# Performance work log

Measured on AMD Instinct MI355X. Metric: run time of the kernel, lower is better.

The kernel has to match this reference:

```python
import jax, jax.numpy as jnp
import numpy as np

KEY_DIM = 128
TEMPERATURE = float(np.sqrt(KEY_DIM))


def setup_inputs() -> dict:
    key = jax.random.key(0)
    kq, kk, kv = jax.random.split(key, 3)
    B, S, D = 32, 2048, KEY_DIM
    q = jax.random.normal(kq, (B, S, D), dtype=jnp.float32)
    k = jax.random.normal(kk, (B, S, D), dtype=jnp.float32)
    v = jax.random.normal(kv, (B, S, D), dtype=jnp.float32)
    return {"q": q, "k": k, "v": v}


def reference(q, k, v):
    # energies: [B, S, S] = q @ k^T / sqrt(D)
    energies = jnp.einsum("bqd,bkd->bqk", q, k) / TEMPERATURE
    S = energies.shape[1]
    # causal mask: disallow attending to future positions (strict upper triangle)
    causal = jnp.tril(jnp.ones((S, S), dtype=bool))
    energies = jnp.where(causal[None, :, :], energies, -jnp.inf)
    attention = jax.nn.softmax(energies, axis=2)  # dropout p=0 -> identity
    context = jnp.einsum("bqk,bkd->bqd", attention, v)
    return (context, attention)
```

## Files before the change

kernel.cpp:

```cpp
#include <hip/hip_runtime.h>


#define BATCH 32
#define SEQ 2048
#define DIM 128
#define BQ 64
#define NT 32
#define NTHREADS 256
#define SCALE 0.08838834764831845f

typedef __attribute__((ext_vector_type(8))) short short8;
typedef __attribute__((ext_vector_type(4))) short short4v;
typedef __attribute__((ext_vector_type(4))) float floatx4;

#define QP 136
#define PP 72

__device__ __forceinline__ short f2bf(float x) {
  unsigned u = __builtin_bit_cast(unsigned, x);
  u += 0x7fffu + ((u >> 16) & 1u);
  return (short)(u >> 16);
}
__device__ __forceinline__ float bf2f(short s) {
  return __builtin_bit_cast(float, (unsigned)(unsigned short)s << 16);
}

__device__ __forceinline__ void stage_f32(const float* __restrict__ g,
                                          short* __restrict__ lds, int tid) {
  int r = tid >> 2, c0 = tid & 3;
  const float* grow = g + r * DIM;
  short* lrow = lds + r * QP;
#pragma unroll
  for (int i = 0; i < 8; ++i) {
    int dq = c0 + 4 * i;
    floatx4 val = *(const floatx4*)(grow + dq * 4);
    short4v o;
    o.x = f2bf(val.x); o.y = f2bf(val.y); o.z = f2bf(val.z); o.w = f2bf(val.w);
    *(short4v*)(lrow + dq * 4) = o;
  }
}
__device__ __forceinline__ void stage_vT_f32(const float* __restrict__ g,
                                             short* __restrict__ lds, int tid) {
  int r = tid >> 2, c0 = tid & 3;
  const float* grow = g + r * DIM;
#pragma unroll
  for (int i = 0; i < 8; ++i) {
    int dq = c0 + 4 * i;
    floatx4 val = *(const floatx4*)(grow + dq * 4);
    lds[(dq * 4 + 0) * PP + r] = f2bf(val.x);
    lds[(dq * 4 + 1) * PP + r] = f2bf(val.y);
    lds[(dq * 4 + 2) * PP + r] = f2bf(val.z);
    lds[(dq * 4 + 3) * PP + r] = f2bf(val.w);
  }
}
__device__ __forceinline__ void load_k_regs(const short* __restrict__ src,
                                            int tid, short8* kr) {
#pragma unroll
  for (int i = 0; i < 4; ++i) {
    int idx = tid + i * 256;
    int r = idx >> 4, g = idx & 15;
    kr[i] = *(const short8*)(src + r * DIM + g * 8);
  }
}
__device__ __forceinline__ void write_k_regs(const short8* kr,
                                             short* __restrict__ ks, int tid) {
#pragma unroll
  for (int i = 0; i < 4; ++i) {
    int idx = tid + i * 256;
    int r = idx >> 4, g = idx & 15;
    *(short8*)(ks + r * QP + g * 8) = kr[i];
  }
}
__device__ __forceinline__ void load_v_regs(const short* __restrict__ src,
                                            int tid, short8* vr) {
#pragma unroll
  for (int i = 0; i < 4; ++i) {
    int idx = tid + i * 256;
    int d = idx >> 3, g = idx & 7;
    vr[i] = *(const short8*)(src + (size_t)d * SEQ + g * 8);
  }
}
__device__ __forceinline__ void write_v_regs(const short8* vr,
                                             short* __restrict__ vts, int tid) {
#pragma unroll
  for (int i = 0; i < 4; ++i) {
    int idx = tid + i * 256;
    int d = idx >> 3, g = idx & 7;
    *(short8*)(vts + d * PP + g * 8) = vr[i];
  }
}

__global__ __launch_bounds__(NTHREADS) void convert_kv(
    const float* __restrict__ k, const float* __restrict__ v,
    short* __restrict__ kbf, short* __restrict__ vbf) {
  int blk = blockIdx.x, tid = threadIdx.x;
  if (blk < BATCH * NT) {
    __shared__ short vt[DIM * PP];
    int b = blk >> 5, s0 = (blk & 31) * BQ;
    const float* src = v + ((size_t)b * SEQ + s0) * DIM;
    int r = tid >> 2, c0 = tid & 3;
#pragma unroll
    for (int i = 0; i < 8; ++i) {
      int dq = c0 + 4 * i;
      floatx4 val = *(const floatx4*)(src + (size_t)r * DIM + dq * 4);
      vt[(dq * 4 + 0) * PP + r] = f2bf(val.x);
      vt[(dq * 4 + 1) * PP + r] = f2bf(val.y);
      vt[(dq * 4 + 2) * PP + r] = f2bf(val.z);
      vt[(dq * 4 + 3) * PP + r] = f2bf(val.w);
    }
    __syncthreads();
#pragma unroll
    for (int i = 0; i < 4; ++i) {
      int idx = tid + i * 256;
      int d = idx >> 3, g = idx & 7;
      *(short8*)(vbf + ((size_t)b * DIM + d) * SEQ + s0 + g * 8) =
          *(const short8*)(vt + d * PP + g * 8);
    }
  } else {
    size_t base = (size_t)(blk - BATCH * NT) * 4096;
    const floatx4* src = (const floatx4*)k;
#pragma unroll
    for (int i = 0; i < 16; ++i) {
      size_t idx = base + i * 256 + tid;
      floatx4 val = src[idx];
      short4v o;
      o.x = f2bf(val.x); o.y = f2bf(val.y); o.z = f2bf(val.z); o.w = f2bf(val.w);
      *(short4v*)(kbf + idx * 4) = o;
    }
  }
}

template <bool PRE>
__global__ __launch_bounds__(NTHREADS, 2) void attn_fused(
    const float* __restrict__ q, const float* __restrict__ k,
    const float* __restrict__ v, const short* __restrict__ kbf,
    const short* __restrict__ vbf, float* __restrict__ ctx,
    float* __restrict__ attn) {
  __shared__ short ks[BQ * QP];
  __shared__ short rest[18432];
  short* vts = rest;
  short* psA = rest + DIM * PP;
  short* psB = psA + BQ * PP;

  const int tid = threadIdx.x;
  const int i = blockIdx.x;
  const int xcd = i & 7;
  const int jj = i >> 3;
  const int b = xcd + 8 * (jj >> 4);
  const int pr = jj & 15;
  const int qtA = pr, qtB = 31 - pr;

  const float* qbase = q + (size_t)b * SEQ * DIM;
  const short* kb = PRE ? kbf + (size_t)b * SEQ * DIM : nullptr;
  const short* vb = PRE ? vbf + (size_t)b * DIM * SEQ : nullptr;
  const float* kbase = k + (size_t)b * SEQ * DIM;
  const float* vbase = v + (size_t)b * SEQ * DIM;
  float* ctxA = ctx + ((size_t)b * SEQ + qtA * BQ) * DIM;
  float* ctxB = ctx + ((size_t)b * SEQ + qtB * BQ) * DIM;
  float* attnA = attn + ((size_t)b * SEQ + qtA * BQ) * SEQ;
  float* attnB = attn + ((size_t)b * SEQ + qtB * BQ) * SEQ;

  stage_f32(qbase + (size_t)qtA * BQ * DIM, rest, tid);
  stage_f32(qbase + (size_t)qtB * BQ * DIM, rest + BQ * QP, tid);

  const int lane = tid & 63;
  const int w = tid >> 6;
  const int quad = lane >> 4;
  const int c = lane & 15;

  __syncthreads();
  short8 afA[4], afB[4];
  {
    const short* ra = rest + (w * 16 + c) * QP + quad * 8;
    const short* rb = ra + BQ * QP;
#pragma unroll
    for (int kk = 0; kk < 4; ++kk) {
      afA[kk] = *(const short8*)(ra + kk * 32);
      afB[kk] = *(const short8*)(rb + kk * 32);
    }
  }

  const int lrow_lo = w * 16 + quad * 4;
  const int nIt = qtB + 1;
  const int zcA = (qtA + 1) * BQ, nzA4 = (SEQ - zcA) >> 2;
  const int zcB = (qtB + 1) * BQ, nzB4 = (SEQ - zcB) >> 2;
  const floatx4 z4 = {0.f, 0.f, 0.f, 0.f};

  float plA[4] = {0.f, 0.f, 0.f, 0.f}, plB[4] = {0.f, 0.f, 0.f, 0.f};
  if (PRE) {
    short8 kr[4];
    load_k_regs(kb, tid, kr);
    write_k_regs(kr, ks, tid);
  } else {
    stage_f32(kbase, ks, tid);
  }
  __syncthreads();
  for (int kt = 0; kt < nIt; ++kt) {
    short* cur = (kt & 1) ? rest : ks;
    short* nxt = (kt & 1) ? ks : rest;
    const bool more = (kt + 1 < nIt);
    short8 kr[4];
    if (PRE && more) load_k_regs(kb + (size_t)(kt + 1) * BQ * DIM, tid, kr);

    const bool activeA = (kt <= qtA);
    const bool diagB = (kt == qtB), diagA = (kt == qtA);
#pragma unroll
    for (int nt = 0; nt < 4; ++nt) {
      const short* brow = cur + (nt * 16 + c) * QP + quad * 8;
      short8 bf[4];
#pragma unroll
      for (int kk = 0; kk < 4; ++kk) bf[kk] = *(const short8*)(brow + kk * 32);
      floatx4 aB = {0.f, 0.f, 0.f, 0.f};
#pragma unroll
      for (int kk = 0; kk < 4; ++kk)
        aB = __builtin_amdgcn_mfma_f32_16x16x32_bf16(afB[kk], bf[kk], aB, 0, 0, 0);
#pragma unroll
      for (int r = 0; r < 4; ++r) {
        bool msk = diagB && (nt * 16 + c > lrow_lo + r);
        plB[r] += msk ? 0.f : __expf(aB[r] * SCALE);
      }
      if (activeA) {
        floatx4 aA = {0.f, 0.f, 0.f, 0.f};
#pragma unroll
        for (int kk = 0; kk < 4; ++kk)
          aA = __builtin_amdgcn_mfma_f32_16x16x32_bf16(afA[kk], bf[kk], aA, 0, 0, 0);
#pragma unroll
        for (int r = 0; r < 4; ++r) {
          bool msk = diagA && (nt * 16 + c > lrow_lo + r);
          plA[r] += msk ? 0.f : __expf(aA[r] * SCALE);
        }
      }
    }

    {
      int r0 = (kt * BQ) / nIt, r1 = ((kt + 1) * BQ) / nIt;
      for (int r = r0; r < r1; ++r) {
        float* rowpA = attnA + (size_t)r * SEQ + zcA;
        for (int c4 = tid; c4 < nzA4; c4 += NTHREADS) *(floatx4*)(rowpA + c4 * 4) = z4;
        float* rowpB = attnB + (size_t)r * SEQ + zcB;
        for (int c4 = tid; c4 < nzB4; c4 += NTHREADS) *(floatx4*)(rowpB + c4 * 4) = z4;
      }
    }

    if (more) {
      if (PRE) write_k_regs(kr, nxt, tid);
      else stage_f32(kbase + (size_t)(kt + 1) * BQ * DIM, nxt, tid);
    }
    __syncthreads();
  }

  float invlA[4], invlB[4];
#pragma unroll
  for (int r = 0; r < 4; ++r) {
#pragma unroll
    for (int off = 1; off < 16; off <<= 1) {
      plA[r] += __shfl_xor(plA[r], off, 16);
      plB[r] += __shfl_xor(plB[r], off, 16);
    }
    invlA[r] = 1.f / plA[r];
    invlB[r] = 1.f / plB[r];
  }

  floatx4 oaccA[8], oaccB[8];
#pragma unroll
  for (int nt = 0; nt < 8; ++nt) { oaccA[nt] = (floatx4)(0.f); oaccB[nt] = (floatx4)(0.f); }

  const short* prowA = psA + (w * 16 + c) * PP + quad * 8;
  const short* prowB = psB + (w * 16 + c) * PP + quad * 8;

  short8 kr2[4], vr2[4];
  if (PRE) { load_k_regs(kb, tid, kr2); load_v_regs(vb, tid, vr2); }
  for (int kt = 0; kt < nIt; ++kt) {
    __syncthreads();
    if (PRE) {
      write_k_regs(kr2, ks, tid);
      write_v_regs(vr2, vts, tid);
    } else {
      stage_f32(kbase + (size_t)kt * BQ * DIM, ks, tid);
      stage_vT_f32(vbase + (size_t)kt * BQ * DIM, vts, tid);
    }
    __syncthreads();
    const bool more = (kt + 1 < nIt);
    if (PRE && more) {
      load_k_regs(kb + (size_t)(kt + 1) * BQ * DIM, tid, kr2);
      load_v_regs(vb + (size_t)(kt + 1) * BQ, tid, vr2);
    }

    const bool activeA = (kt <= qtA);
    const bool diagB = (kt == qtB), diagA = (kt == qtA);
#pragma unroll
    for (int nt = 0; nt < 4; ++nt) {
      const short* brow = ks + (nt * 16 + c) * QP + quad * 8;
      short8 bf[4];
#pragma unroll
      for (int kk = 0; kk < 4; ++kk) bf[kk] = *(const short8*)(brow + kk * 32);
      floatx4 aB = {0.f, 0.f, 0.f, 0.f};
#pragma unroll
      for (int kk = 0; kk < 4; ++kk)
        aB = __builtin_amdgcn_mfma_f32_16x16x32_bf16(afB[kk], bf[kk], aB, 0, 0, 0);
#pragma unroll
      for (int r = 0; r < 4; ++r) {
        bool msk = diagB && (nt * 16 + c > lrow_lo + r);
        float p = msk ? 0.f : __expf(aB[r] * SCALE) * invlB[r];
        psB[(lrow_lo + r) * PP + nt * 16 + c] = f2bf(p);
      }
      if (activeA) {
        floatx4 aA = {0.f, 0.f, 0.f, 0.f};
#pragma unroll
        for (int kk = 0; kk < 4; ++kk)
          aA = __builtin_amdgcn_mfma_f32_16x16x32_bf16(afA[kk], bf[kk], aA, 0, 0, 0);
#pragma unroll
        for (int r = 0; r < 4; ++r) {
          bool msk = diagA && (nt * 16 + c > lrow_lo + r);
          float p = msk ? 0.f : __expf(aA[r] * SCALE) * invlA[r];
          psA[(lrow_lo + r) * PP + nt * 16 + c] = f2bf(p);
        }
      }
    }

#pragma unroll
    for (int ks2 = 0; ks2 < 2; ++ks2) {
      short8 paB = *(const short8*)(prowB + ks2 * 32);
      short8 paA;
      if (activeA) paA = *(const short8*)(prowA + ks2 * 32);
#pragma unroll
      for (int nt = 0; nt < 8; ++nt) {
        short8 vf = *(const short8*)(vts + (nt * 16 + c) * PP + ks2 * 32 + quad * 8);
        oaccB[nt] = __builtin_amdgcn_mfma_f32_16x16x32_bf16(paB, vf, oaccB[nt], 0, 0, 0);
        if (activeA)
          oaccA[nt] = __builtin_amdgcn_mfma_f32_16x16x32_bf16(paA, vf, oaccA[nt], 0, 0, 0);
      }
    }

#pragma unroll
    for (int it = 0; it < 4; ++it) {
      int idx = lane + it * 64;
      int r = (idx >> 4) + w * 16;
      int q4 = idx & 15;
      short4v pb = *(const short4v*)(psB + r * PP + q4 * 4);
      floatx4 fo;
      fo.x = bf2f(pb.x); fo.y = bf2f(pb.y); fo.z = bf2f(pb.z); fo.w = bf2f(pb.w);
      *(floatx4*)(attnB + (size_t)r * SEQ + kt * BQ + q4 * 4) = fo;
      if (activeA) {
        short4v pa = *(const short4v*)(psA + r * PP + q4 * 4);
        floatx4 fa;
        fa.x = bf2f(pa.x); fa.y = bf2f(pa.y); fa.z = bf2f(pa.z); fa.w = bf2f(pa.w);
        *(floatx4*)(attnA + (size_t)r * SEQ + kt * BQ + q4 * 4) = fa;
      }
    }
  }

#pragma unroll
  for (int nt = 0; nt < 8; ++nt)
#pragma unroll
    for (int r = 0; r < 4; ++r) {
      ctxA[(size_t)(lrow_lo + r) * DIM + nt * 16 + c] = oaccA[nt][r];
      ctxB[(size_t)(lrow_lo + r) * DIM + nt * 16 + c] = oaccB[nt][r];
    }
}

extern "C" void kernel_launch(void* const* d_in, const int* in_sizes, int n_in,
                              void* d_out, int out_size, void* d_ws, size_t ws_size,
                              hipStream_t stream) {
  (void)in_sizes; (void)n_in; (void)out_size;
  const float* q = (const float*)d_in[0];
  const float* k = (const float*)d_in[1];
  const float* v = (const float*)d_in[2];
  float* ctx = (float*)d_out;
  float* attn = ctx + (size_t)BATCH * SEQ * DIM;
  const size_t kv_elems = (size_t)BATCH * SEQ * DIM;
  const size_t need = kv_elems * 2 * sizeof(short);
  dim3 grid(BATCH * NT / 2);
  if (ws_size >= need) {
    short* kbf = (short*)d_ws;
    short* vbf = kbf + kv_elems;
    convert_kv<<<dim3(BATCH * NT + 512), NTHREADS, 0, stream>>>(k, v, kbf, vbf);
    attn_fused<true><<<grid, NTHREADS, 0, stream>>>(q, k, v, kbf, vbf, ctx, attn);
  } else {
    attn_fused<false><<<grid, NTHREADS, 0, stream>>>(q, k, v, nullptr, nullptr, ctx, attn);
  }
}
```

Baseline: 710.5 us.

## Read bf16 K/V fragments directly from global memory instead of staging through LDS

The precomputed-bf16 path becomes its own kernel that loads MFMA B-operand fragments for K and transposed V straight from global memory (relying on L2/cache), instead of cooperatively staging each tile into shared memory. This removes the per-tile __syncthreads barriers and LDS write traffic, and shrinks shared memory to the Q and probability buffers. The attention-matrix and context outputs now use nontemporal stores. The trade-off is redundant global/cache loads across the four waves with less coalesced access, plus exposed load latency that is no longer hidden by explicit prefetch.

```diff
diff --git a/kernel.cpp b/kernel.cpp
--- a/kernel.cpp
+++ b/kernel.cpp
@@ -51,42 +51,6 @@
     lds[(dq * 4 + 1) * PP + r] = f2bf(val.y);
     lds[(dq * 4 + 2) * PP + r] = f2bf(val.z);
     lds[(dq * 4 + 3) * PP + r] = f2bf(val.w);
-  }
-}
-__device__ __forceinline__ void load_k_regs(const short* __restrict__ src,
-                                            int tid, short8* kr) {
-#pragma unroll
-  for (int i = 0; i < 4; ++i) {
-    int idx = tid + i * 256;
-    int r = idx >> 4, g = idx & 15;
-    kr[i] = *(const short8*)(src + r * DIM + g * 8);
-  }
-}
-__device__ __forceinline__ void write_k_regs(const short8* kr,
-                                             short* __restrict__ ks, int tid) {
-#pragma unroll
-  for (int i = 0; i < 4; ++i) {
-    int idx = tid + i * 256;
-    int r = idx >> 4, g = idx & 15;
-    *(short8*)(ks + r * QP + g * 8) = kr[i];
-  }
-}
-__device__ __forceinline__ void load_v_regs(const short* __restrict__ src,
-                                            int tid, short8* vr) {
-#pragma unroll
-  for (int i = 0; i < 4; ++i) {
-    int idx = tid + i * 256;
-    int d = idx >> 3, g = idx & 7;
-    vr[i] = *(const short8*)(src + (size_t)d * SEQ + g * 8);
-  }
-}
-__device__ __forceinline__ void write_v_regs(const short8* vr,
-                                             short* __restrict__ vts, int tid) {
-#pragma unroll
-  for (int i = 0; i < 4; ++i) {
-    int idx = tid + i * 256;
-    int d = idx >> 3, g = idx & 7;
-    *(short8*)(vts + d * PP + g * 8) = vr[i];
   }
 }
 
@@ -130,17 +94,13 @@
   }
 }
 
-template <bool PRE>
-__global__ __launch_bounds__(NTHREADS, 2) void attn_fused(
-    const float* __restrict__ q, const float* __restrict__ k,
-    const float* __restrict__ v, const short* __restrict__ kbf,
+__global__ __launch_bounds__(NTHREADS, 2) void attn_pre(
+    const float* __restrict__ q, const short* __restrict__ kbf,
     const short* __restrict__ vbf, float* __restrict__ ctx,
     float* __restrict__ attn) {
-  __shared__ short ks[BQ * QP];
-  __shared__ short rest[18432];
-  short* vts = rest;
-  short* psA = rest + DIM * PP;
-  short* psB = psA + BQ * PP;
+  __shared__ short qs[2 * BQ * QP];
+  __shared__ short psA[BQ * PP];
+  __shared__ short psB[BQ * PP];
 
   const int tid = threadIdx.x;
   const int i = blockIdx.x;
@@ -151,8 +111,205 @@
   const int qtA = pr, qtB = 31 - pr;
 
   const float* qbase = q + (size_t)b * SEQ * DIM;
-  const short* kb = PRE ? kbf + (size_t)b * SEQ * DIM : nullptr;
-  const short* vb = PRE ? vbf + (size_t)b * DIM * SEQ : nullptr;
+  const short* kb = kbf + (size_t)b * SEQ * DIM;
+  const short* vb = vbf + (size_t)b * DIM * SEQ;
+  float* ctxA = ctx + ((size_t)b * SEQ + qtA * BQ) * DIM;
+  float* ctxB = ctx + ((size_t)b * SEQ + qtB * BQ) * DIM;
+  float* attnA = attn + ((size_t)b * SEQ + qtA * BQ) * SEQ;
+  float* attnB = attn + ((size_t)b * SEQ + qtB * BQ) * SEQ;
+
+  stage_f32(qbase + (size_t)qtA * BQ * DIM, qs, tid);
+  stage_f32(qbase + (size_t)qtB * BQ * DIM, qs + BQ * QP, tid);
+
+  const int lane = tid & 63;
+  const int w = tid >> 6;
+  const int quad = lane >> 4;
+  const int c = lane & 15;
+
+  __syncthreads();
+  short8 afA[4], afB[4];
+  {
+    const short* ra = qs + (w * 16 + c) * QP + quad * 8;
+    const short* rb = ra + BQ * QP;
+#pragma unroll
+    for (int kk = 0; kk < 4; ++kk) {
+      afA[kk] = *(const short8*)(ra + kk * 32);
+      afB[kk] = *(const short8*)(rb + kk * 32);
+    }
+  }
+
+  const int lrow_lo = w * 16 + quad * 4;
+  const int nIt = qtB + 1;
+  const int zcA = (qtA + 1) * BQ, nzA4 = (SEQ - zcA) >> 2;
+  const int zcB = (qtB + 1) * BQ, nzB4 = (SEQ - zcB) >> 2;
+  const floatx4 z4 = {0.f, 0.f, 0.f, 0.f};
+
+  float plA[4] = {0.f, 0.f, 0.f, 0.f}, plB[4] = {0.f, 0.f, 0.f, 0.f};
+  for (int kt = 0; kt < nIt; ++kt) {
+    const short* kg = kb + (size_t)kt * BQ * DIM;
+    const bool activeA = (kt <= qtA);
+    const bool diagB = (kt == qtB), diagA = (kt == qtA);
+#pragma unroll
+    for (int nt = 0; nt < 4; ++nt) {
+      const short* brow = kg + (nt * 16 + c) * DIM + quad * 8;
+      short8 bf[4];
+#pragma unroll
+      for (int kk = 0; kk < 4; ++kk) bf[kk] = *(const short8*)(brow + kk * 32);
+      floatx4 aB = {0.f, 0.f, 0.f, 0.f};
+#pragma unroll
+      for (int kk = 0; kk < 4; ++kk)
+        aB = __builtin_amdgcn_mfma_f32_16x16x32_bf16(afB[kk], bf[kk], aB, 0, 0, 0);
+#pragma unroll
+      for (int r = 0; r < 4; ++r) {
+        bool msk = diagB && (nt * 16 + c > lrow_lo + r);
+        plB[r] += msk ? 0.f : __expf(aB[r] * SCALE);
+      }
+      if (activeA) {
+        floatx4 aA = {0.f, 0.f, 0.f, 0.f};
+#pragma unroll
+        for (int kk = 0; kk < 4; ++kk)
+          aA = __builtin_amdgcn_mfma_f32_16x16x32_bf16(afA[kk], bf[kk], aA, 0, 0, 0);
+#pragma unroll
+        for (int r = 0; r < 4; ++r) {
+          bool msk = diagA && (nt * 16 + c > lrow_lo + r);
+          plA[r] += msk ? 0.f : __expf(aA[r] * SCALE);
+        }
+      }
+    }
+    {
+      int r0 = (kt * BQ) / nIt, r1 = ((kt + 1) * BQ) / nIt;
+      for (int r = r0; r < r1; ++r) {
+        float* rowpA = attnA + (size_t)r * SEQ + zcA;
+        for (int c4 = tid; c4 < nzA4; c4 += NTHREADS)
+          __builtin_nontemporal_store(z4, (floatx4*)(rowpA + c4 * 4));
+        float* rowpB = attnB + (size_t)r * SEQ + zcB;
+        for (int c4 = tid; c4 < nzB4; c4 += NTHREADS)
+          __builtin_nontemporal_store(z4, (floatx4*)(rowpB + c4 * 4));
+      }
+    }
+  }
+
+  float invlA[4], invlB[4];
+#pragma unroll
+  for (int r = 0; r < 4; ++r) {
+#pragma unroll
+    for (int off = 1; off < 16; off <<= 1) {
+      plA[r] += __shfl_xor(plA[r], off, 16);
+      plB[r] += __shfl_xor(plB[r], off, 16);
+    }
+    invlA[r] = 1.f / plA[r];
+    invlB[r] = 1.f / plB[r];
+  }
+
+  floatx4 oaccA[8], oaccB[8];
+#pragma unroll
+  for (int nt = 0; nt < 8; ++nt) { oaccA[nt] = (floatx4)(0.f); oaccB[nt] = (floatx4)(0.f); }
+
+  const short* prowA = psA + (w * 16 + c) * PP + quad * 8;
+  const short* prowB = psB + (w * 16 + c) * PP + quad * 8;
+
+  for (int kt = 0; kt < nIt; ++kt) {
+    const short* kg = kb + (size_t)kt * BQ * DIM;
+    const bool activeA = (kt <= qtA);
+    const bool diagB = (kt == qtB), diagA = (kt == qtA);
+#pragma unroll
+    for (int nt = 0; nt < 4; ++nt) {
+      const short* brow = kg + (nt * 16 + c) * DIM + quad * 8;
+      short8 bf[4];
+#pragma unroll
+      for (int kk = 0; kk < 4; ++kk) bf[kk] = *(const short8*)(brow + kk * 32);
+      floatx4 aB = {0.f, 0.f, 0.f, 0.f};
+#pragma unroll
+      for (int kk = 0; kk < 4; ++kk)
+        aB = __builtin_amdgcn_mfma_f32_16x16x32_bf16(afB[kk], bf[kk], aB, 0, 0, 0);
+#pragma unroll
+      for (int r = 0; r < 4; ++r) {
+        bool msk = diagB && (nt * 16 + c > lrow_lo + r);
+        float p = msk ? 0.f : __expf(aB[r] * SCALE) * invlB[r];
+        psB[(lrow_lo + r) * PP + nt * 16 + c] = f2bf(p);
+      }
+      if (activeA) {
+        floatx4 aA = {0.f, 0.f, 0.f, 0.f};
+#pragma unroll
+        for (int kk = 0; kk < 4; ++kk)
+          aA = __builtin_amdgcn_mfma_f32_16x16x32_bf16(afA[kk], bf[kk], aA, 0, 0, 0);
+#pragma unroll
+        for (int r = 0; r < 4; ++r) {
+          bool msk = diagA && (nt * 16 + c > lrow_lo + r);
+          float p = msk ? 0.f : __expf(aA[r] * SCALE) * invlA[r];
+          psA[(lrow_lo + r) * PP + nt * 16 + c] = f2bf(p);
+        }
+      }
+    }
+
+    const short* vg = vb + (size_t)kt * BQ;
+#pragma unroll
+    for (int ks2 = 0; ks2 < 2; ++ks2) {
+      short8 paB = *(const short8*)(prowB + ks2 * 32);
+      short8 paA;
+      if (activeA) paA = *(const short8*)(prowA + ks2 * 32);
+#pragma unroll
+      for (int nt = 0; nt < 8; ++nt) {
+        short8 vf = *(const short8*)(vg + (size_t)(nt * 16 + c) * SEQ + ks2 * 32 + quad * 8);
+        oaccB[nt] = __builtin_amdgcn_mfma_f32_16x16x32_bf16(paB, vf, oaccB[nt], 0, 0, 0);
+        if (activeA)
+          oaccA[nt] = __builtin_amdgcn_mfma_f32_16x16x32_bf16(paA, vf, oaccA[nt], 0, 0, 0);
+      }
+    }
+
+#pragma unroll
+    for (int it2 = 0; it2 < 2; ++it2) {
+      int rl = it2 * 8 + (lane >> 3), g = lane & 7;
+      int r = w * 16 + rl;
+      short8 pb = *(const short8*)(psB + r * PP + g * 8);
+      floatx4 lo, hi;
+      lo.x = bf2f(pb[0]); lo.y = bf2f(pb[1]); lo.z = bf2f(pb[2]); lo.w = bf2f(pb[3]);
+      hi.x = bf2f(pb[4]); hi.y = bf2f(pb[5]); hi.z = bf2f(pb[6]); hi.w = bf2f(pb[7]);
+      float* dst = attnB + (size_t)r * SEQ + kt * BQ + g * 8;
+      __builtin_nontemporal_store(lo, (floatx4*)dst);
+      __builtin_nontemporal_store(hi, (floatx4*)(dst + 4));
+      if (activeA) {
+        short8 pa = *(const short8*)(psA + r * PP + g * 8);
+        floatx4 lo2, hi2;
+        lo2.x = bf2f(pa[0]); lo2.y = bf2f(pa[1]); lo2.z = bf2f(pa[2]); lo2.w = bf2f(pa[3]);
+        hi2.x = bf2f(pa[4]); hi2.y = bf2f(pa[5]); hi2.z = bf2f(pa[6]); hi2.w = bf2f(pa[7]);
+        float* dstA = attnA + (size_t)r * SEQ + kt * BQ + g * 8;
+        __builtin_nontemporal_store(lo2, (floatx4*)dstA);
+        __builtin_nontemporal_store(hi2, (floatx4*)(dstA + 4));
+      }
+    }
+  }
+
+#pragma unroll
+  for (int nt = 0; nt < 8; ++nt)
+#pragma unroll
+    for (int r = 0; r < 4; ++r) {
+      __builtin_nontemporal_store(oaccA[nt][r],
+          ctxA + (size_t)(lrow_lo + r) * DIM + nt * 16 + c);
+      __builtin_nontemporal_store(oaccB[nt][r],
+          ctxB + (size_t)(lrow_lo + r) * DIM + nt * 16 + c);
+    }
+}
+
+__global__ __launch_bounds__(NTHREADS, 2) void attn_fallback(
+    const float* __restrict__ q, const float* __restrict__ k,
+    const float* __restrict__ v, float* __restrict__ ctx,
+    float* __restrict__ attn) {
+  __shared__ short ks[BQ * QP];
+  __shared__ short rest[18432];
+  short* vts = rest;
+  short* psA = rest + DIM * PP;
+  short* psB = psA + BQ * PP;
+
+  const int tid = threadIdx.x;
+  const int i = blockIdx.x;
+  const int xcd = i & 7;
+  const int jj = i >> 3;
+  const int b = xcd + 8 * (jj >> 4);
+  const int pr = jj & 15;
+  const int qtA = pr, qtB = 31 - pr;
+
+  const float* qbase = q + (size_t)b * SEQ * DIM;
   const float* kbase = k + (size_t)b * SEQ * DIM;
   const float* vbase = v + (size_t)b * SEQ * DIM;
   float* ctxA = ctx + ((size_t)b * SEQ + qtA * BQ) * DIM;
@@ -187,21 +344,12 @@
   const floatx4 z4 = {0.f, 0.f, 0.f, 0.f};
 
   float plA[4] = {0.f, 0.f, 0.f, 0.f}, plB[4] = {0.f, 0.f, 0.f, 0.f};
-  if (PRE) {
-    short8 kr[4];
-    load_k_regs(kb, tid, kr);
-    write_k_regs(kr, ks, tid);
-  } else {
-    stage_f32(kbase, ks, tid);
-  }
+  stage_f32(kbase, ks, tid);
   __syncthreads();
   for (int kt = 0; kt < nIt; ++kt) {
     short* cur = (kt & 1) ? rest : ks;
     short* nxt = (kt & 1) ? ks : rest;
     const bool more = (kt + 1 < nIt);
-    short8 kr[4];
-    if (PRE && more) load_k_regs(kb + (size_t)(kt + 1) * BQ * DIM, tid, kr);
-
     const bool activeA = (kt <= qtA);
     const bool diagB = (kt == qtB), diagA = (kt == qtA);
 #pragma unroll
@@ -231,7 +379,6 @@
         }
       }
     }
-
     {
       int r0 = (kt * BQ) / nIt, r1 = ((kt + 1) * BQ) / nIt;
       for (int r = r0; r < r1; ++r) {
@@ -241,11 +388,7 @@
         for (int c4 = tid; c4 < nzB4; c4 += NTHREADS) *(floatx4*)(rowpB + c4 * 4) = z4;
       }
     }
-
-    if (more) {
-      if (PRE) write_k_regs(kr, nxt, tid);
-      else stage_f32(kbase + (size_t)(kt + 1) * BQ * DIM, nxt, tid);
-    }
+    if (more) stage_f32(kbase + (size_t)(kt + 1) * BQ * DIM, nxt, tid);
     __syncthreads();
   }
 
@@ -268,23 +411,11 @@
   const short* prowA = psA + (w * 16 + c) * PP + quad * 8;
   const short* prowB = psB + (w * 16 + c) * PP + quad * 8;
 
-  short8 kr2[4], vr2[4];
-  if (PRE) { load_k_regs(kb, tid, kr2); load_v_regs(vb, tid, vr2); }
   for (int kt = 0; kt < nIt; ++kt) {
     __syncthreads();
-    if (PRE) {
-      write_k_regs(kr2, ks, tid);
-      write_v_regs(vr2, vts, tid);
-    } else {
-      stage_f32(kbase + (size_t)kt * BQ * DIM, ks, tid);
-      stage_vT_f32(vbase + (size_t)kt * BQ * DIM, vts, tid);
-    }
+    stage_f32(kbase + (size_t)kt * BQ * DIM, ks, tid);
+    stage_vT_f32(vbase + (size_t)kt * BQ * DIM, vts, tid);
     __syncthreads();
-    const bool more = (kt + 1 < nIt);
-    if (PRE && more) {
-      load_k_regs(kb + (size_t)(kt + 1) * BQ * DIM, tid, kr2);
-      load_v_regs(vb + (size_t)(kt + 1) * BQ, tid, vr2);
-    }
 
     const bool activeA = (kt <= qtA);
     const bool diagB = (kt == qtB), diagA = (kt == qtA);
@@ -375,8 +506,8 @@
     short* kbf = (short*)d_ws;
     short* vbf = kbf + kv_elems;
     convert_kv<<<dim3(BATCH * NT + 512), NTHREADS, 0, stream>>>(k, v, kbf, vbf);
-    attn_fused<true><<<grid, NTHREADS, 0, stream>>>(q, k, v, kbf, vbf, ctx, attn);
+    attn_pre<<<grid, NTHREADS, 0, stream>>>(q, kbf, vbf, ctx, attn);
   } else {
-    attn_fused<false><<<grid, NTHREADS, 0, stream>>>(q, k, v, nullptr, nullptr, ctx, attn);
-  }
-}
+    attn_fallback<<<grid, NTHREADS, 0, stream>>>(q, k, v, ctx, attn);
+  }
+}
```

Result: slower. 888.5 us (+25.1%).
